# Kernel tuning notes

Measured on AMD Instinct MI355X. Metric: run time of the kernel, lower is better.

The kernel has to match this reference:

```python
import jax, jax.numpy as jnp
import numpy as np

B, T, V, E, H, NT = 64, 512, 8000, 256, 512, 4
HD = H // 2  # hidden per direction


def setup_inputs() -> dict:
    key = jax.random.key(0)
    ks = jax.random.split(key, 14)
    s = 0.1
    length = jnp.sort(jax.random.randint(ks[0], (B,), T // 2, T + 1))[::-1]  # sorted desc (pack_padded)
    mask = (jnp.arange(T)[None, :] < length[:, None]).astype(jnp.int32)
    sentence = jax.random.randint(ks[1], (B, T), 1, V + 1) * mask  # pad positions -> padding_idx 0
    tags = jax.random.randint(ks[2], (B, T), 0, NT)
    embedding = (jax.random.normal(ks[3], (V + 1, E)) * s).at[0].set(0.0)  # padding_idx row = 0
    w_ih_f = jax.random.normal(ks[4], (4 * HD, E)) * s
    w_hh_f = jax.random.normal(ks[5], (4 * HD, HD)) * s
    b_f = jax.random.normal(ks[6], (4 * HD,)) * s  # b_ih + b_hh combined
    w_ih_b = jax.random.normal(ks[7], (4 * HD, E)) * s
    w_hh_b = jax.random.normal(ks[8], (4 * HD, HD)) * s
    b_b = jax.random.normal(ks[9], (4 * HD,)) * s
    w_out = jax.random.normal(ks[10], (NT, H)) * s
    b_out = jnp.zeros((NT,), jnp.float32)
    start_trans = jax.random.uniform(ks[11], (NT,), minval=-0.1, maxval=0.1)
    end_trans = jax.random.uniform(ks[12], (NT,), minval=-0.1, maxval=0.1)
    trans = jax.random.uniform(ks[13], (NT, NT), minval=-0.1, maxval=0.1)
    return {"sentence": sentence, "tags": tags, "mask": mask, "length": length,
            "embedding": embedding, "w_ih_f": w_ih_f, "w_hh_f": w_hh_f, "b_f": b_f,
            "w_ih_b": w_ih_b, "w_hh_b": w_hh_b, "b_b": b_b,
            "w_out": w_out, "b_out": b_out,
            "start_trans": start_trans, "end_trans": end_trans, "trans": trans}


def _lstm_dir(x, maskf, w_ih, w_hh, b, reverse):
    # x: [B,T,E]; masked LSTM == packed LSTM (zero init state, padded outputs = 0)
    xg = jnp.einsum('bte,ge->btg', x, w_ih) + b           # [B,T,4HD]
    xg = jnp.swapaxes(xg, 0, 1)                           # [T,B,4HD]
    mt = jnp.swapaxes(maskf, 0, 1)[..., None]             # [T,B,1]
    h0 = jnp.zeros((x.shape[0], w_hh.shape[1]), x.dtype)

    def step(carry, inp):
        h, c = carry
        g, m = inp
        gates = g + h @ w_hh.T
        i, f, gg, o = jnp.split(gates, 4, axis=-1)  # torch gate order: i, f, g, o
        i = jax.nn.sigmoid(i); f = jax.nn.sigmoid(f)
        gg = jnp.tanh(gg); o = jax.nn.sigmoid(o)
        cn = f * c + i * gg
        hn = o * jnp.tanh(cn)
        h = m * hn + (1.0 - m) * h
        c = m * cn + (1.0 - m) * c
        return (h, c), h * m

    _, hs = jax.lax.scan(step, (h0, h0), (xg, mt), reverse=reverse)
    return jnp.swapaxes(hs, 0, 1)  # [B,T,HD]


def reference(sentence, tags, mask, length, embedding, w_ih_f, w_hh_f, b_f,
              w_ih_b, w_hh_b, b_b, w_out, b_out, start_trans, end_trans, trans):
    maskf = mask.astype(embedding.dtype)
    embeds = embedding[sentence]                           # [B,T,E] (dropout: eval/identity)
    hf = _lstm_dir(embeds, maskf, w_ih_f, w_hh_f, b_f, False)
    hb = _lstm_dir(embeds, maskf, w_ih_b, w_hh_b, b_b, True)
    feats = jnp.concatenate([hf, hb], -1) @ w_out.T + b_out  # [B,T,NT]

    # --- CRF log-likelihood (torchcrf), reduction='mean'; loss = -mean llh ---
    bsz = tags.shape[0]
    emit = jnp.take_along_axis(feats, tags[..., None], -1)[..., 0]   # [B,T]
    trans_sc = trans[tags[:, :-1], tags[:, 1:]]                       # [B,T-1]
    num = start_trans[tags[:, 0]] + emit[:, 0] \
        + jnp.sum(maskf[:, 1:] * (emit[:, 1:] + trans_sc), axis=1)
    last_tag = tags[jnp.arange(bsz), length - 1]
    num = num + end_trans[last_tag]

    ft = jnp.swapaxes(feats, 0, 1)                  # [T,B,NT]
    mt = jnp.swapaxes(maskf, 0, 1)[..., None]       # [T,B,1]
    alpha0 = start_trans[None, :] + ft[0]

    def step(alpha, inp):
        e, m = inp
        new = jax.nn.logsumexp(alpha[:, :, None] + trans[None] + e[:, None, :], axis=1)
        return m * new + (1.0 - m) * alpha, None

    alpha, _ = jax.lax.scan(step, alpha0, (ft[1:], mt[1:]))
    logZ = jax.nn.logsumexp(alpha + end_trans[None, :], axis=1)
    return -jnp.mean(num - logZ)
```

## Files before the change

### kernel.cpp

```cpp
#include <hip/hip_runtime.h>
#include <stdint.h>

#define BB 64
#define TT 512
#define EE 256
#define NTAG 4

typedef _Float16 f16;
typedef _Float16 half8 __attribute__((ext_vector_type(8)));
typedef _Float16 f16x4 __attribute__((ext_vector_type(4)));
typedef float floatx4 __attribute__((ext_vector_type(4)));

__device__ __forceinline__ int dot4i8(uint32_t a, uint32_t b, int c) {
#if __has_builtin(__builtin_amdgcn_sdot4)
  return __builtin_amdgcn_sdot4((int)a, (int)b, c, false);
#else
  int r;
  asm("v_dot4_i32_i8 %0, %1, %2, %3" : "=v"(r) : "v"(a), "v"(b), "v"(c));
  return r;
#endif
}

__device__ __forceinline__ float sigm(float x) {
  x = fminf(fmaxf(x, -30.f), 30.f);
  return 1.f / (1.f + __expf(-x));
}
__device__ __forceinline__ float tanh_f(float x) {
  x = fminf(fmaxf(x, -15.f), 15.f);
  float e = __expf(-2.f * x);
  return (1.f - e) / (1.f + e);
}

__global__ void pack_kernel(const float* __restrict__ wihf, const float* __restrict__ wihb,
                            const float* __restrict__ whhf, const float* __restrict__ whhb,
                            f16* __restrict__ bmat, uint32_t* __restrict__ whhp,
                            float* __restrict__ swhh) {
  int wv = (blockIdx.x * 256 + threadIdx.x) >> 6;
  int lane = threadIdx.x & 63;
  if (wv >= 2048) return;
  int dir = wv >> 10;
  int outr = wv & 1023;
  int srcg = (outr & 3) * 256 + (outr >> 2);
  const float* wih = dir ? wihb : wihf;
  const float* src = wih + (size_t)srcg * EE + lane * 4;
  f16* bp = bmat + (size_t)wv * EE + lane * 4;
  floatx4 v = *(const floatx4*)src;
  bp[0] = (f16)v[0]; bp[1] = (f16)v[1]; bp[2] = (f16)v[2]; bp[3] = (f16)v[3];
  int g = outr;
  const float* whh = dir ? whhb : whhf;
  floatx4 w = *(const floatx4*)(whh + (size_t)g * EE + lane * 4);
  float am = fmaxf(fmaxf(fabsf(w[0]), fabsf(w[1])), fmaxf(fabsf(w[2]), fabsf(w[3])));
#pragma unroll
  for (int d = 1; d < 64; d <<= 1) am = fmaxf(am, __shfl_xor(am, d));
  float s = am * (1.f / 127.f);
  float inv = am > 0.f ? 127.f / am : 0.f;
  int q0 = (int)rintf(w[0] * inv);
  int q1 = (int)rintf(w[1] * inv);
  int q2 = (int)rintf(w[2] * inv);
  int q3 = (int)rintf(w[3] * inv);
  uint32_t p = (uint32_t)(q0 & 255) | ((uint32_t)(q1 & 255) << 8) |
               ((uint32_t)(q2 & 255) << 16) | ((uint32_t)(q3 & 255) << 24);
  whhp[dir * 65536 + lane * 1024 + g] = p;
  if (lane == 0) swhh[dir * 1024 + g] = s;
}

__global__ __launch_bounds__(256) void gemm_kernel(
    const int* __restrict__ sentence, const float* __restrict__ embedding,
    const f16* __restrict__ bmat, f16* __restrict__ xgF, f16* __restrict__ xgB,
    int t0f, int t0b, int L, int Lsh) {
  __shared__ __attribute__((aligned(16))) f16 As[128][72];
  __shared__ __attribute__((aligned(16))) f16 Bs[128][72];
  int rt = blockIdx.x;
  int nt = blockIdx.y;
  int tid = threadIdx.x;
  int lane = tid & 63;
  int wv = tid >> 6;
  int BL = BB * L;
  int rbase = rt * 128;
  int half = (rbase >= BL) ? 1 : 0;
  int rloc0 = rbase - half * BL;
  int t0 = half ? t0b : t0f;

  floatx4 acc[4][4];
#pragma unroll
  for (int i = 0; i < 4; ++i)
#pragma unroll
    for (int j = 0; j < 4; ++j) acc[i][j] = (floatx4){0.f, 0.f, 0.f, 0.f};

  int ar = tid >> 1;
  int part = tid & 1;
  int rl = rloc0 + ar;
  int b_ = rl >> Lsh;
  int dt = rl & (L - 1);
  int t_ = t0 + dt;
  int sidx = sentence[b_ * TT + t_];
  const float* arow = embedding + (size_t)sidx * EE + part * 32;
  const f16* brow = bmat + ((size_t)(half * 1024 + nt * 128 + ar)) * EE + part * 32;
  int wm = (wv >> 1) * 64, wn = (wv & 1) * 64;

  for (int kk = 0; kk < 4; ++kk) {
    int k0 = kk * 64;
#pragma unroll
    for (int i = 0; i < 4; ++i) {
      floatx4 a0 = *(const floatx4*)(arow + k0 + i * 8);
      floatx4 a1 = *(const floatx4*)(arow + k0 + i * 8 + 4);
      union { f16 h[8]; uint4 u; } cv;
      cv.h[0] = (f16)a0[0]; cv.h[1] = (f16)a0[1]; cv.h[2] = (f16)a0[2]; cv.h[3] = (f16)a0[3];
      cv.h[4] = (f16)a1[0]; cv.h[5] = (f16)a1[1]; cv.h[6] = (f16)a1[2]; cv.h[7] = (f16)a1[3];
      *(uint4*)(&As[ar][part * 32 + i * 8]) = cv.u;
    }
#pragma unroll
    for (int i = 0; i < 4; ++i) {
      uint4 bv = *(const uint4*)(brow + k0 + i * 8);
      *(uint4*)(&Bs[ar][part * 32 + i * 8]) = bv;
    }
    __syncthreads();
#pragma unroll
    for (int kf = 0; kf < 2; ++kf) {
      int ko = kf * 32 + (lane >> 4) * 8;
      half8 af[4], bf[4];
#pragma unroll
      for (int mi = 0; mi < 4; ++mi)
        af[mi] = *(const half8*)(&As[wm + mi * 16 + (lane & 15)][ko]);
#pragma unroll
      for (int ni = 0; ni < 4; ++ni)
        bf[ni] = *(const half8*)(&Bs[wn + ni * 16 + (lane & 15)][ko]);
#pragma unroll
      for (int mi = 0; mi < 4; ++mi)
#pragma unroll
        for (int ni = 0; ni < 4; ++ni)
          acc[mi][ni] = __builtin_amdgcn_mfma_f32_16x16x32_f16(af[mi], bf[ni], acc[mi][ni], 0, 0, 0);
    }
    __syncthreads();
  }
  f16* out = half ? xgB : xgF;
#pragma unroll
  for (int mi = 0; mi < 4; ++mi) {
#pragma unroll
    for (int ni = 0; ni < 4; ++ni) {
      int rowl = wm + mi * 16 + (lane >> 4) * 4;
      int coll = nt * 128 + wn + ni * 16 + (lane & 15);
#pragma unroll
      for (int r = 0; r < 4; ++r) {
        out[(size_t)(rloc0 + rowl + r) * 1024 + coll] = (f16)acc[mi][ni][r];
      }
    }
  }
}

__global__ __launch_bounds__(256, 1) void rec_kernel(
    const int* __restrict__ length, const f16* __restrict__ xgF, const f16* __restrict__ xgB,
    const uint32_t* __restrict__ whhp, const float* __restrict__ swhh,
    const float* __restrict__ b_f, const float* __restrict__ b_b,
    f16* __restrict__ hsF, f16* __restrict__ hsB,
    float* __restrict__ hstate, float* __restrict__ cstate,
    int t0f, int t0b, int L, int first) {
  __shared__ __attribute__((aligned(16))) uint32_t hq4[2][64];
  int wid = blockIdx.x;
  int b = wid >> 1, dir = wid & 1;
  int j = threadIdx.x;
  int len = length[b];

  const uint32_t* wp = whhp + dir * 65536;
  uint32_t wr0[64], wr1[64], wr2[64], wr3[64];
#pragma unroll
  for (int q = 0; q < 64; ++q) {
    wr0[q] = wp[q * 1024 + j];
    wr1[q] = wp[q * 1024 + 256 + j];
    wr2[q] = wp[q * 1024 + 512 + j];
    wr3[q] = wp[q * 1024 + 768 + j];
  }
  const float* sb = swhh + dir * 1024;
  float sw0 = sb[j] * (1.f / 127.f), sw1 = sb[256 + j] * (1.f / 127.f);
  float sw2 = sb[512 + j] * (1.f / 127.f), sw3 = sb[768 + j] * (1.f / 127.f);
  const float* bias = dir ? b_b : b_f;
  float bi0 = bias[j], bi1 = bias[256 + j], bi2 = bias[512 + j], bi3 = bias[768 + j];

  float h = 0.f, c = 0.f;
  if (!first) {
    h = hstate[(dir * BB + b) * 256 + j];
    c = cstate[(dir * BB + b) * 256 + j];
  }
  const f16* xg = dir ? xgB : xgF;
  f16* hs = dir ? hsB : hsF;

  int qi = (int)rintf(h * 127.f);
  qi = max(-127, min(127, qi));
  ((uint8_t*)&hq4[0][0])[j] = (uint8_t)qi;
  __syncthreads();

  int tlo = dir ? t0b : t0f;
  int thi = min(tlo + L, len);
  int nsteps = thi - tlo;
  int p = 0;
  for (int ii = 0; ii < nsteps; ++ii) {
    int t = dir ? (thi - 1 - ii) : (tlo + ii);
    f16x4 xv = *(const f16x4*)(xg + (((size_t)(b * L + (t - tlo))) << 10) + j * 4);
    int A00 = 0, A01 = 0, A10 = 0, A11 = 0, A20 = 0, A21 = 0, A30 = 0, A31 = 0;
#pragma unroll
    for (int k = 0; k < 16; ++k) {
      uint4 v = *((const uint4*)&hq4[p][0] + k);
      A00 = dot4i8(wr0[4 * k + 0], v.x, A00); A01 = dot4i8(wr0[4 * k + 1], v.y, A01);
      A00 = dot4i8(wr0[4 * k + 2], v.z, A00); A01 = dot4i8(wr0[4 * k + 3], v.w, A01);
      A10 = dot4i8(wr1[4 * k + 0], v.x, A10); A11 = dot4i8(wr1[4 * k + 1], v.y, A11);
      A10 = dot4i8(wr1[4 * k + 2], v.z, A10); A11 = dot4i8(wr1[4 * k + 3], v.w, A11);
      A20 = dot4i8(wr2[4 * k + 0], v.x, A20); A21 = dot4i8(wr2[4 * k + 1], v.y, A21);
      A20 = dot4i8(wr2[4 * k + 2], v.z, A20); A21 = dot4i8(wr2[4 * k + 3], v.w, A21);
      A30 = dot4i8(wr3[4 * k + 0], v.x, A30); A31 = dot4i8(wr3[4 * k + 1], v.y, A31);
      A30 = dot4i8(wr3[4 * k + 2], v.z, A30); A31 = dot4i8(wr3[4 * k + 3], v.w, A31);
    }
    float pi = (float)xv[0] + bi0 + sw0 * (float)(A00 + A01);
    float pf = (float)xv[1] + bi1 + sw1 * (float)(A10 + A11);
    float pg = (float)xv[2] + bi2 + sw2 * (float)(A20 + A21);
    float po = (float)xv[3] + bi3 + sw3 * (float)(A30 + A31);
    float iv = sigm(pi), fv = sigm(pf), gv = tanh_f(pg), ov = sigm(po);
    c = fv * c + iv * gv;
    h = ov * tanh_f(c);
    hs[(((size_t)(b * TT + t)) << 8) + j] = (f16)h;
    int q = (int)rintf(h * 127.f);
    q = max(-127, min(127, q));
    ((uint8_t*)&hq4[p ^ 1][0])[j] = (uint8_t)q;
    __syncthreads();
    p ^= 1;
  }
  hstate[(dir * BB + b) * 256 + j] = h;
  cstate[(dir * BB + b) * 256 + j] = c;
}

__global__ __launch_bounds__(256) void feats_kernel(
    const f16* __restrict__ hsF, const f16* __restrict__ hsB,
    const float* __restrict__ w_out, const float* __restrict__ b_out,
    float* __restrict__ feats) {
  int gw = (blockIdx.x * 256 + threadIdx.x) >> 6;
  int lane = threadIdx.x & 63;
  int nw = (gridDim.x * 256) >> 6;
  float w0[8], w1[8], w2[8], w3[8];
#pragma unroll
  for (int u = 0; u < 8; ++u) {
    w0[u] = w_out[0 * 512 + lane * 8 + u];
    w1[u] = w_out[1 * 512 + lane * 8 + u];
    w2[u] = w_out[2 * 512 + lane * 8 + u];
    w3[u] = w_out[3 * 512 + lane * 8 + u];
  }
  float bo0 = b_out[0], bo1 = b_out[1], bo2 = b_out[2], bo3 = b_out[3];
  const f16* src0 = (lane < 32) ? (hsF + lane * 8) : (hsB + (lane - 32) * 8);
  for (int row = gw; row < BB * TT; row += nw) {
    union { uint4 u; f16 h[8]; } hv;
    hv.u = *(const uint4*)(src0 + ((size_t)row << 8));
    float a0 = 0.f, a1 = 0.f, a2 = 0.f, a3 = 0.f;
#pragma unroll
    for (int u2 = 0; u2 < 8; ++u2) {
      float x = (float)hv.h[u2];
      a0 += x * w0[u2]; a1 += x * w1[u2]; a2 += x * w2[u2]; a3 += x * w3[u2];
    }
#pragma unroll
    for (int d = 1; d < 64; d <<= 1) {
      a0 += __shfl_xor(a0, d); a1 += __shfl_xor(a1, d);
      a2 += __shfl_xor(a2, d); a3 += __shfl_xor(a3, d);
    }
    if (lane == 0) {
      floatx4 o = {a0 + bo0, a1 + bo1, a2 + bo2, a3 + bo3};
      *(floatx4*)(feats + (size_t)row * 4) = o;
    }
  }
}

__global__ void crf_kernel(const int* __restrict__ tags, const int* __restrict__ length,
                           const float* __restrict__ feats,
                           const float* __restrict__ start_trans,
                           const float* __restrict__ end_trans, const float* __restrict__ trans,
                           float* __restrict__ res) {
  int b = blockIdx.x;
  int lane = threadIdx.x;
  int len = length[b];
  float tr0 = lane < 4 ? trans[0 * 4 + lane] : 0.f;
  float tr1 = lane < 4 ? trans[1 * 4 + lane] : 0.f;
  float tr2 = lane < 4 ? trans[2 * 4 + lane] : 0.f;
  float tr3 = lane < 4 ? trans[3 * 4 + lane] : 0.f;
  float treg = lane < 16 ? trans[lane] : 0.f;
  float st = lane < 4 ? start_trans[lane] : 0.f;
  float en = lane < 4 ? end_trans[lane] : 0.f;
  const int* tg = tags + b * TT;
  const float* fb = feats + (size_t)b * TT * 4;

  float e = lane < 4 ? fb[lane] : 0.f;
  int prev = tg[0];
  float alpha = st + e;
  float num = __shfl(st + e, prev);
#pragma unroll 2
  for (int t = 1; t < len; ++t) {
    float et = lane < 4 ? fb[t * 4 + lane] : 0.f;
    int cur = tg[t];
    float a0 = __shfl(alpha, 0), a1 = __shfl(alpha, 1), a2 = __shfl(alpha, 2), a3 = __shfl(alpha, 3);
    float v0 = a0 + tr0, v1 = a1 + tr1, v2 = a2 + tr2, v3 = a3 + tr3;
    float mx = fmaxf(fmaxf(v0, v1), fmaxf(v2, v3));
    float sm = __expf(v0 - mx) + __expf(v1 - mx) + __expf(v2 - mx) + __expf(v3 - mx);
    alpha = mx + __logf(sm) + et;
    num += __shfl(et, cur) + __shfl(treg, prev * 4 + cur);
    prev = cur;
  }
  num += __shfl(en, prev);
  float v = alpha + en;
  float z0 = __shfl(v, 0), z1 = __shfl(v, 1), z2 = __shfl(v, 2), z3 = __shfl(v, 3);
  float mx = fmaxf(fmaxf(z0, z1), fmaxf(z2, z3));
  float logZ = mx + __logf(__expf(z0 - mx) + __expf(z1 - mx) + __expf(z2 - mx) + __expf(z3 - mx));
  if (lane == 0) res[b] = num - logZ;
}

__global__ void loss_kernel(const float* __restrict__ res, float* __restrict__ out) {
  int lane = threadIdx.x;
  float v = res[lane];
#pragma unroll
  for (int d = 1; d < 64; d <<= 1) v += __shfl_xor(v, d);
  if (lane == 0) out[0] = -v * (1.f / 64.f);
}

extern "C" void kernel_launch(void* const* d_in, const int* in_sizes, int n_in,
                              void* d_out, int out_size, void* d_ws, size_t ws_size,
                              hipStream_t stream) {
  (void)in_sizes; (void)n_in; (void)out_size;
  const int* sentence = (const int*)d_in[0];
  const int* tags = (const int*)d_in[1];
  const int* length = (const int*)d_in[3];
  const float* embedding = (const float*)d_in[4];
  const float* w_ih_f = (const float*)d_in[5];
  const float* w_hh_f = (const float*)d_in[6];
  const float* b_f = (const float*)d_in[7];
  const float* w_ih_b = (const float*)d_in[8];
  const float* w_hh_b = (const float*)d_in[9];
  const float* b_b = (const float*)d_in[10];
  const float* w_out = (const float*)d_in[11];
  const float* b_out = (const float*)d_in[12];
  const float* start_trans = (const float*)d_in[13];
  const float* end_trans = (const float*)d_in[14];
  const float* trans = (const float*)d_in[15];

  char* ws = (char*)d_ws;
  size_t off = 0;
  auto take = [&](size_t bytes) -> char* {
    char* p = ws + off;
    off = (off + bytes + 255) & ~(size_t)255;
    return p;
  };
  f16* bmat = (f16*)take((size_t)2048 * 256 * 2);
  uint32_t* whhp = (uint32_t*)take((size_t)2 * 64 * 1024 * 4);
  float* swhh = (float*)take((size_t)2 * 1024 * 4);
  f16* hsF = (f16*)take((size_t)BB * TT * 256 * 2);
  f16* hsB = (f16*)take((size_t)BB * TT * 256 * 2);
  float* feats = (float*)take((size_t)BB * TT * NTAG * 4);
  float* hstate = (float*)take((size_t)2 * BB * 256 * 4);
  float* cstate = (float*)take((size_t)2 * BB * 256 * 4);
  float* res = (float*)take(256);
  size_t fixed = off;

  int L = TT, Lsh = 9;
  while (L > 32 && fixed + (size_t)BB * L * 1024 * 2 * 2 > ws_size) { L >>= 1; Lsh--; }
  f16* xgF = (f16*)take((size_t)BB * L * 1024 * 2);
  f16* xgB = (f16*)take((size_t)BB * L * 1024 * 2);
  int NC = TT / L;

  hipLaunchKernelGGL(pack_kernel, dim3(512), dim3(256), 0, stream,
                     w_ih_f, w_ih_b, w_hh_f, w_hh_b, bmat, whhp, swhh);

  for (int cidx = 0; cidx < NC; ++cidx) {
    int t0f_ = cidx * L;
    int t0b_ = TT - (cidx + 1) * L;
    hipLaunchKernelGGL(gemm_kernel, dim3(2 * BB * L / 128, 8), dim3(256), 0, stream,
                       sentence, embedding, bmat, xgF, xgB, t0f_, t0b_, L, Lsh);
    hipLaunchKernelGGL(rec_kernel, dim3(128), dim3(256), 0, stream,
                       length, xgF, xgB, whhp, swhh, b_f, b_b, hsF, hsB,
                       hstate, cstate, t0f_, t0b_, L, cidx == 0 ? 1 : 0);
  }
  hipLaunchKernelGGL(feats_kernel, dim3(512), dim3(256), 0, stream,
                     hsF, hsB, w_out, b_out, feats);
  hipLaunchKernelGGL(crf_kernel, dim3(BB), dim3(64), 0, stream,
                     tags, length, feats, start_trans, end_trans, trans, res);
  hipLaunchKernelGGL(loss_kernel, dim3(1), dim3(64), 0, stream, res, (float*)d_out);
}
```

Measured before the change: 1.126 ms.

## Park recurrent weights in AGPRs and prefetch next-step input gates

```diff
diff --git a/kernel.cpp b/kernel.cpp
--- a/kernel.cpp
+++ b/kernel.cpp
@@ -8,7 +8,6 @@
 
 typedef _Float16 f16;
 typedef _Float16 half8 __attribute__((ext_vector_type(8)));
-typedef _Float16 f16x4 __attribute__((ext_vector_type(4)));
 typedef float floatx4 __attribute__((ext_vector_type(4)));
 
 __device__ __forceinline__ int dot4i8(uint32_t a, uint32_t b, int c) {
@@ -39,14 +38,12 @@
   int lane = threadIdx.x & 63;
   if (wv >= 2048) return;
   int dir = wv >> 10;
-  int outr = wv & 1023;
-  int srcg = (outr & 3) * 256 + (outr >> 2);
+  int g = wv & 1023;
   const float* wih = dir ? wihb : wihf;
-  const float* src = wih + (size_t)srcg * EE + lane * 4;
+  const float* src = wih + (size_t)g * EE + lane * 4;
   f16* bp = bmat + (size_t)wv * EE + lane * 4;
   floatx4 v = *(const floatx4*)src;
   bp[0] = (f16)v[0]; bp[1] = (f16)v[1]; bp[2] = (f16)v[2]; bp[3] = (f16)v[3];
-  int g = outr;
   const float* whh = dir ? whhb : whhf;
   floatx4 w = *(const floatx4*)(whh + (size_t)g * EE + lane * 4);
   float am = fmaxf(fmaxf(fabsf(w[0]), fabsf(w[1])), fmaxf(fabsf(w[2]), fabsf(w[3])));
@@ -85,7 +82,7 @@
 #pragma unroll
   for (int i = 0; i < 4; ++i)
 #pragma unroll
-    for (int j = 0; j < 4; ++j) acc[i][j] = (floatx4){0.f, 0.f, 0.f, 0.f};
+    for (int j2 = 0; j2 < 4; ++j2) acc[i][j2] = (floatx4){0.f, 0.f, 0.f, 0.f};
 
   int ar = tid >> 1;
   int part = tid & 1;
@@ -147,6 +144,58 @@
     }
   }
 }
+
+#define PARK4(c0, c1, c2, c3) \
+  uint32_t awI_##c0, awF_##c0, awG_##c0, awO_##c0; \
+  uint32_t awI_##c1, awF_##c1, awG_##c1, awO_##c1; \
+  uint32_t awI_##c2, awF_##c2, awG_##c2, awO_##c2; \
+  uint32_t awI_##c3, awF_##c3, awG_##c3, awO_##c3; \
+  { uint32_t xI0 = wp[(c0)*1024 + j],       xF0 = wp[(c0)*1024 + 256 + j]; \
+    uint32_t xG0 = wp[(c0)*1024 + 512 + j], xO0 = wp[(c0)*1024 + 768 + j]; \
+    uint32_t xI1 = wp[(c1)*1024 + j],       xF1 = wp[(c1)*1024 + 256 + j]; \
+    uint32_t xG1 = wp[(c1)*1024 + 512 + j], xO1 = wp[(c1)*1024 + 768 + j]; \
+    uint32_t xI2 = wp[(c2)*1024 + j],       xF2 = wp[(c2)*1024 + 256 + j]; \
+    uint32_t xG2 = wp[(c2)*1024 + 512 + j], xO2 = wp[(c2)*1024 + 768 + j]; \
+    uint32_t xI3 = wp[(c3)*1024 + j],       xF3 = wp[(c3)*1024 + 256 + j]; \
+    uint32_t xG3 = wp[(c3)*1024 + 512 + j], xO3 = wp[(c3)*1024 + 768 + j]; \
+    asm volatile("v_accvgpr_write_b32 %0, %1" : "=a"(awI_##c0) : "v"(xI0)); \
+    asm volatile("v_accvgpr_write_b32 %0, %1" : "=a"(awF_##c0) : "v"(xF0)); \
+    asm volatile("v_accvgpr_write_b32 %0, %1" : "=a"(awG_##c0) : "v"(xG0)); \
+    asm volatile("v_accvgpr_write_b32 %0, %1" : "=a"(awO_##c0) : "v"(xO0)); \
+    asm volatile("v_accvgpr_write_b32 %0, %1" : "=a"(awI_##c1) : "v"(xI1)); \
+    asm volatile("v_accvgpr_write_b32 %0, %1" : "=a"(awF_##c1) : "v"(xF1)); \
+    asm volatile("v_accvgpr_write_b32 %0, %1" : "=a"(awG_##c1) : "v"(xG1)); \
+    asm volatile("v_accvgpr_write_b32 %0, %1" : "=a"(awO_##c1) : "v"(xO1)); \
+    asm volatile("v_accvgpr_write_b32 %0, %1" : "=a"(awI_##c2) : "v"(xI2)); \
+    asm volatile("v_accvgpr_write_b32 %0, %1" : "=a"(awF_##c2) : "v"(xF2)); \
+    asm volatile("v_accvgpr_write_b32 %0, %1" : "=a"(awG_##c2) : "v"(xG2)); \
+    asm volatile("v_accvgpr_write_b32 %0, %1" : "=a"(awO_##c2) : "v"(xO2)); \
+    asm volatile("v_accvgpr_write_b32 %0, %1" : "=a"(awI_##c3) : "v"(xI3)); \
+    asm volatile("v_accvgpr_write_b32 %0, %1" : "=a"(awF_##c3) : "v"(xF3)); \
+    asm volatile("v_accvgpr_write_b32 %0, %1" : "=a"(awG_##c3) : "v"(xG3)); \
+    asm volatile("v_accvgpr_write_b32 %0, %1" : "=a"(awO_##c3) : "v"(xO3)); }
+
+#define RDW(nm) asm volatile("v_accvgpr_read_b32 %0, %1" : "=v"(w) : "a"(nm))
+
+#define DOTQ(q, c0, c1, c2, c3) { \
+  uint4 hv = hqcur[q]; \
+  uint32_t w; \
+  RDW(awI_##c0); Ai0 = dot4i8(w, hv.x, Ai0); \
+  RDW(awI_##c1); Ai1 = dot4i8(w, hv.y, Ai1); \
+  RDW(awI_##c2); Ai0 = dot4i8(w, hv.z, Ai0); \
+  RDW(awI_##c3); Ai1 = dot4i8(w, hv.w, Ai1); \
+  RDW(awF_##c0); Af0 = dot4i8(w, hv.x, Af0); \
+  RDW(awF_##c1); Af1 = dot4i8(w, hv.y, Af1); \
+  RDW(awF_##c2); Af0 = dot4i8(w, hv.z, Af0); \
+  RDW(awF_##c3); Af1 = dot4i8(w, hv.w, Af1); \
+  RDW(awG_##c0); Ag0 = dot4i8(w, hv.x, Ag0); \
+  RDW(awG_##c1); Ag1 = dot4i8(w, hv.y, Ag1); \
+  RDW(awG_##c2); Ag0 = dot4i8(w, hv.z, Ag0); \
+  RDW(awG_##c3); Ag1 = dot4i8(w, hv.w, Ag1); \
+  RDW(awO_##c0); Ao0 = dot4i8(w, hv.x, Ao0); \
+  RDW(awO_##c1); Ao1 = dot4i8(w, hv.y, Ao1); \
+  RDW(awO_##c2); Ao0 = dot4i8(w, hv.z, Ao0); \
+  RDW(awO_##c3); Ao1 = dot4i8(w, hv.w, Ao1); }
 
 __global__ __launch_bounds__(256, 1) void rec_kernel(
     const int* __restrict__ length, const f16* __restrict__ xgF, const f16* __restrict__ xgB,
@@ -162,19 +211,16 @@
   int len = length[b];
 
   const uint32_t* wp = whhp + dir * 65536;
-  uint32_t wr0[64], wr1[64], wr2[64], wr3[64];
-#pragma unroll
-  for (int q = 0; q < 64; ++q) {
-    wr0[q] = wp[q * 1024 + j];
-    wr1[q] = wp[q * 1024 + 256 + j];
-    wr2[q] = wp[q * 1024 + 512 + j];
-    wr3[q] = wp[q * 1024 + 768 + j];
-  }
+  PARK4(0, 1, 2, 3)     PARK4(4, 5, 6, 7)     PARK4(8, 9, 10, 11)   PARK4(12, 13, 14, 15)
+  PARK4(16, 17, 18, 19) PARK4(20, 21, 22, 23) PARK4(24, 25, 26, 27) PARK4(28, 29, 30, 31)
+  PARK4(32, 33, 34, 35) PARK4(36, 37, 38, 39) PARK4(40, 41, 42, 43) PARK4(44, 45, 46, 47)
+  PARK4(48, 49, 50, 51) PARK4(52, 53, 54, 55) PARK4(56, 57, 58, 59) PARK4(60, 61, 62, 63)
+
   const float* sb = swhh + dir * 1024;
-  float sw0 = sb[j] * (1.f / 127.f), sw1 = sb[256 + j] * (1.f / 127.f);
-  float sw2 = sb[512 + j] * (1.f / 127.f), sw3 = sb[768 + j] * (1.f / 127.f);
+  float swI = sb[j] * (1.f / 127.f), swF = sb[256 + j] * (1.f / 127.f);
+  float swG = sb[512 + j] * (1.f / 127.f), swO = sb[768 + j] * (1.f / 127.f);
   const float* bias = dir ? b_b : b_f;
-  float bi0 = bias[j], bi1 = bias[256 + j], bi2 = bias[512 + j], bi3 = bias[768 + j];
+  float biI = bias[j], biF = bias[256 + j], biG = bias[512 + j], biO = bias[768 + j];
 
   float h = 0.f, c = 0.f;
   if (!first) {
@@ -192,36 +238,43 @@
   int tlo = dir ? t0b : t0f;
   int thi = min(tlo + L, len);
   int nsteps = thi - tlo;
-  int p = 0;
+  int pp = 0;
+  int r0 = b * L + (dir ? (thi - 1 - tlo) : 0);
+  int sgn = dir ? -1 : 1;
+  f16 xI_c = (f16)0.f, xF_c = (f16)0.f, xG_c = (f16)0.f, xO_c = (f16)0.f;
+  if (nsteps > 0) {
+    const f16* xrow = xg + (((size_t)r0) << 10);
+    xI_c = xrow[j]; xF_c = xrow[256 + j]; xG_c = xrow[512 + j]; xO_c = xrow[768 + j];
+  }
   for (int ii = 0; ii < nsteps; ++ii) {
-    int t = dir ? (thi - 1 - ii) : (tlo + ii);
-    f16x4 xv = *(const f16x4*)(xg + (((size_t)(b * L + (t - tlo))) << 10) + j * 4);
-    int A00 = 0, A01 = 0, A10 = 0, A11 = 0, A20 = 0, A21 = 0, A30 = 0, A31 = 0;
-#pragma unroll
-    for (int k = 0; k < 16; ++k) {
-      uint4 v = *((const uint4*)&hq4[p][0] + k);
-      A00 = dot4i8(wr0[4 * k + 0], v.x, A00); A01 = dot4i8(wr0[4 * k + 1], v.y, A01);
-      A00 = dot4i8(wr0[4 * k + 2], v.z, A00); A01 = dot4i8(wr0[4 * k + 3], v.w, A01);
-      A10 = dot4i8(wr1[4 * k + 0], v.x, A10); A11 = dot4i8(wr1[4 * k + 1], v.y, A11);
-      A10 = dot4i8(wr1[4 * k + 2], v.z, A10); A11 = dot4i8(wr1[4 * k + 3], v.w, A11);
-      A20 = dot4i8(wr2[4 * k + 0], v.x, A20); A21 = dot4i8(wr2[4 * k + 1], v.y, A21);
-      A20 = dot4i8(wr2[4 * k + 2], v.z, A20); A21 = dot4i8(wr2[4 * k + 3], v.w, A21);
-      A30 = dot4i8(wr3[4 * k + 0], v.x, A30); A31 = dot4i8(wr3[4 * k + 1], v.y, A31);
-      A30 = dot4i8(wr3[4 * k + 2], v.z, A30); A31 = dot4i8(wr3[4 * k + 3], v.w, A31);
-    }
-    float pi = (float)xv[0] + bi0 + sw0 * (float)(A00 + A01);
-    float pf = (float)xv[1] + bi1 + sw1 * (float)(A10 + A11);
-    float pg = (float)xv[2] + bi2 + sw2 * (float)(A20 + A21);
-    float po = (float)xv[3] + bi3 + sw3 * (float)(A30 + A31);
+    f16 xI_n = xI_c, xF_n = xF_c, xG_n = xG_c, xO_n = xO_c;
+    if (ii + 1 < nsteps) {
+      const f16* xrow = xg + (((size_t)(r0 + sgn * (ii + 1))) << 10);
+      xI_n = xrow[j]; xF_n = xrow[256 + j]; xG_n = xrow[512 + j]; xO_n = xrow[768 + j];
+    }
+    const uint4* hqcur = (const uint4*)&hq4[pp][0];
+    int Ai0 = 0, Ai1 = 0, Af0 = 0, Af1 = 0, Ag0 = 0, Ag1 = 0, Ao0 = 0, Ao1 = 0;
+    DOTQ(0, 0, 1, 2, 3)     DOTQ(1, 4, 5, 6, 7)     DOTQ(2, 8, 9, 10, 11)
+    DOTQ(3, 12, 13, 14, 15) DOTQ(4, 16, 17, 18, 19) DOTQ(5, 20, 21, 22, 23)
+    DOTQ(6, 24, 25, 26, 27) DOTQ(7, 28, 29, 30, 31) DOTQ(8, 32, 33, 34, 35)
+    DOTQ(9, 36, 37, 38, 39) DOTQ(10, 40, 41, 42, 43) DOTQ(11, 44, 45, 46, 47)
+    DOTQ(12, 48, 49, 50, 51) DOTQ(13, 52, 53, 54, 55) DOTQ(14, 56, 57, 58, 59)
+    DOTQ(15, 60, 61, 62, 63)
+    float pi = (float)xI_c + biI + swI * (float)(Ai0 + Ai1);
+    float pf = (float)xF_c + biF + swF * (float)(Af0 + Af1);
+    float pg = (float)xG_c + biG + swG * (float)(Ag0 + Ag1);
+    float po = (float)xO_c + biO + swO * (float)(Ao0 + Ao1);
     float iv = sigm(pi), fv = sigm(pf), gv = tanh_f(pg), ov = sigm(po);
     c = fv * c + iv * gv;
     h = ov * tanh_f(c);
-    hs[(((size_t)(b * TT + t)) << 8) + j] = (f16)h;
+    int tt = dir ? (thi - 1 - ii) : (tlo + ii);
+    hs[(((size_t)(b * TT + tt)) << 8) + j] = (f16)h;
     int q = (int)rintf(h * 127.f);
     q = max(-127, min(127, q));
-    ((uint8_t*)&hq4[p ^ 1][0])[j] = (uint8_t)q;
+    ((uint8_t*)&hq4[pp ^ 1][0])[j] = (uint8_t)q;
     __syncthreads();
-    p ^= 1;
+    pp ^= 1;
+    xI_c = xI_n; xF_c = xF_n; xG_c = xG_n; xO_c = xO_n;
   }
   hstate[(dir * BB + b) * 256 + j] = h;
   cstate[(dir * BB + b) * 256 + j] = c;
```

Measured after the change: 1.181 ms. 1.05x slower.

## Split each LSTM recurrence across two peer blocks with flag-based hidden exchange

Applied to the files above, without the earlier changes.

```diff
diff --git a/kernel.cpp b/kernel.cpp
--- a/kernel.cpp
+++ b/kernel.cpp
@@ -8,7 +8,6 @@
 
 typedef _Float16 f16;
 typedef _Float16 half8 __attribute__((ext_vector_type(8)));
-typedef _Float16 f16x4 __attribute__((ext_vector_type(4)));
 typedef float floatx4 __attribute__((ext_vector_type(4)));
 
 __device__ __forceinline__ int dot4i8(uint32_t a, uint32_t b, int c) {
@@ -34,19 +33,21 @@
 __global__ void pack_kernel(const float* __restrict__ wihf, const float* __restrict__ wihb,
                             const float* __restrict__ whhf, const float* __restrict__ whhb,
                             f16* __restrict__ bmat, uint32_t* __restrict__ whhp,
-                            float* __restrict__ swhh) {
+                            float* __restrict__ swhh, uint32_t* __restrict__ fl) {
+  if (blockIdx.x == 0) {
+    fl[threadIdx.x] = 0;
+    fl[256 + threadIdx.x] = 0;
+  }
   int wv = (blockIdx.x * 256 + threadIdx.x) >> 6;
   int lane = threadIdx.x & 63;
   if (wv >= 2048) return;
   int dir = wv >> 10;
-  int outr = wv & 1023;
-  int srcg = (outr & 3) * 256 + (outr >> 2);
+  int g = wv & 1023;
   const float* wih = dir ? wihb : wihf;
-  const float* src = wih + (size_t)srcg * EE + lane * 4;
+  const float* src = wih + (size_t)g * EE + lane * 4;
   f16* bp = bmat + (size_t)wv * EE + lane * 4;
   floatx4 v = *(const floatx4*)src;
   bp[0] = (f16)v[0]; bp[1] = (f16)v[1]; bp[2] = (f16)v[2]; bp[3] = (f16)v[3];
-  int g = outr;
   const float* whh = dir ? whhb : whhf;
   floatx4 w = *(const floatx4*)(whh + (size_t)g * EE + lane * 4);
   float am = fmaxf(fmaxf(fabsf(w[0]), fabsf(w[1])), fmaxf(fabsf(w[2]), fabsf(w[3])));
@@ -85,7 +86,7 @@
 #pragma unroll
   for (int i = 0; i < 4; ++i)
 #pragma unroll
-    for (int j = 0; j < 4; ++j) acc[i][j] = (floatx4){0.f, 0.f, 0.f, 0.f};
+    for (int j2 = 0; j2 < 4; ++j2) acc[i][j2] = (floatx4){0.f, 0.f, 0.f, 0.f};
 
   int ar = tid >> 1;
   int part = tid & 1;
@@ -148,83 +149,166 @@
   }
 }
 
+#define LDWO(k)  uint32_t wa##k = wpAo[(k)*1024];      uint32_t wb##k = wpBo[(k)*1024];
+#define LDWX(k)  uint32_t wa##k = wpAx[((k)-32)*1024]; uint32_t wb##k = wpBx[((k)-32)*1024];
+
+#define DOTQ4(k0,k1,k2,k3,HV) { uint4 hv = (HV); \
+  aA0 = dot4i8(wa##k0, hv.x, aA0); aA1 = dot4i8(wa##k1, hv.y, aA1); \
+  aA0 = dot4i8(wa##k2, hv.z, aA0); aA1 = dot4i8(wa##k3, hv.w, aA1); \
+  aB0 = dot4i8(wb##k0, hv.x, aB0); aB1 = dot4i8(wb##k1, hv.y, aB1); \
+  aB0 = dot4i8(wb##k2, hv.z, aB0); aB1 = dot4i8(wb##k3, hv.w, aB1); }
+
 __global__ __launch_bounds__(256, 1) void rec_kernel(
     const int* __restrict__ length, const f16* __restrict__ xgF, const f16* __restrict__ xgB,
     const uint32_t* __restrict__ whhp, const float* __restrict__ swhh,
     const float* __restrict__ b_f, const float* __restrict__ b_b,
     f16* __restrict__ hsF, f16* __restrict__ hsB,
     float* __restrict__ hstate, float* __restrict__ cstate,
+    uint32_t* __restrict__ hx, uint32_t* __restrict__ fl,
     int t0f, int t0b, int L, int first) {
-  __shared__ __attribute__((aligned(16))) uint32_t hq4[2][64];
-  int wid = blockIdx.x;
-  int b = wid >> 1, dir = wid & 1;
-  int j = threadIdx.x;
+  __shared__ __attribute__((aligned(16))) uint32_t hqd[64];
+  __shared__ float gbuf[128], obuf[128];
+
+  int bid = blockIdx.x;
+  int side = bid >> 7;
+  int sub = bid & 127;
+  int b = sub >> 1, dir = sub & 1;
+  int peer = bid ^ 128;
+  int tid = threadIdx.x;
+  int tl = tid & 127;
+  int grp = tid >> 7;
+  int dabs = side * 128 + tl;
+  int rowA = grp * 512 + dabs;
+  int rowB = rowA + 256;
   int len = length[b];
 
-  const uint32_t* wp = whhp + dir * 65536;
-  uint32_t wr0[64], wr1[64], wr2[64], wr3[64];
-#pragma unroll
-  for (int q = 0; q < 64; ++q) {
-    wr0[q] = wp[q * 1024 + j];
-    wr1[q] = wp[q * 1024 + 256 + j];
-    wr2[q] = wp[q * 1024 + 512 + j];
-    wr3[q] = wp[q * 1024 + 768 + j];
-  }
-  const float* sb = swhh + dir * 1024;
-  float sw0 = sb[j] * (1.f / 127.f), sw1 = sb[256 + j] * (1.f / 127.f);
-  float sw2 = sb[512 + j] * (1.f / 127.f), sw3 = sb[768 + j] * (1.f / 127.f);
+  const uint32_t* wpbase = whhp + dir * 65536;
+  const uint32_t* wpAo = wpbase + rowA + (size_t)(side * 32) * 1024;
+  const uint32_t* wpAx = wpbase + rowA + (size_t)((side ^ 1) * 32) * 1024;
+  const uint32_t* wpBo = wpbase + rowB + (size_t)(side * 32) * 1024;
+  const uint32_t* wpBx = wpbase + rowB + (size_t)((side ^ 1) * 32) * 1024;
+  LDWO(0)  LDWO(1)  LDWO(2)  LDWO(3)  LDWO(4)  LDWO(5)  LDWO(6)  LDWO(7)
+  LDWO(8)  LDWO(9)  LDWO(10) LDWO(11) LDWO(12) LDWO(13) LDWO(14) LDWO(15)
+  LDWO(16) LDWO(17) LDWO(18) LDWO(19) LDWO(20) LDWO(21) LDWO(22) LDWO(23)
+  LDWO(24) LDWO(25) LDWO(26) LDWO(27) LDWO(28) LDWO(29) LDWO(30) LDWO(31)
+  LDWX(32) LDWX(33) LDWX(34) LDWX(35) LDWX(36) LDWX(37) LDWX(38) LDWX(39)
+  LDWX(40) LDWX(41) LDWX(42) LDWX(43) LDWX(44) LDWX(45) LDWX(46) LDWX(47)
+  LDWX(48) LDWX(49) LDWX(50) LDWX(51) LDWX(52) LDWX(53) LDWX(54) LDWX(55)
+  LDWX(56) LDWX(57) LDWX(58) LDWX(59) LDWX(60) LDWX(61) LDWX(62) LDWX(63)
+
+  float sA = swhh[dir * 1024 + rowA] * (1.f / 127.f);
+  float sB = swhh[dir * 1024 + rowB] * (1.f / 127.f);
   const float* bias = dir ? b_b : b_f;
-  float bi0 = bias[j], bi1 = bias[256 + j], bi2 = bias[512 + j], bi3 = bias[768 + j];
+  float bA = bias[rowA], bB = bias[rowB];
 
   float h = 0.f, c = 0.f;
-  if (!first) {
-    h = hstate[(dir * BB + b) * 256 + j];
-    c = cstate[(dir * BB + b) * 256 + j];
+  if (!first && tid < 128) {
+    h = hstate[(dir * BB + b) * 256 + dabs];
+    c = cstate[(dir * BB + b) * 256 + dabs];
   }
   const f16* xg = dir ? xgB : xgF;
   f16* hs = dir ? hsB : hsF;
-
-  int qi = (int)rintf(h * 127.f);
-  qi = max(-127, min(127, qi));
-  ((uint8_t*)&hq4[0][0])[j] = (uint8_t)qi;
-  __syncthreads();
 
   int tlo = dir ? t0b : t0f;
   int thi = min(tlo + L, len);
   int nsteps = thi - tlo;
-  int p = 0;
-  for (int ii = 0; ii < nsteps; ++ii) {
-    int t = dir ? (thi - 1 - ii) : (tlo + ii);
-    f16x4 xv = *(const f16x4*)(xg + (((size_t)(b * L + (t - tlo))) << 10) + j * 4);
-    int A00 = 0, A01 = 0, A10 = 0, A11 = 0, A20 = 0, A21 = 0, A30 = 0, A31 = 0;
-#pragma unroll
-    for (int k = 0; k < 16; ++k) {
-      uint4 v = *((const uint4*)&hq4[p][0] + k);
-      A00 = dot4i8(wr0[4 * k + 0], v.x, A00); A01 = dot4i8(wr0[4 * k + 1], v.y, A01);
-      A00 = dot4i8(wr0[4 * k + 2], v.z, A00); A01 = dot4i8(wr0[4 * k + 3], v.w, A01);
-      A10 = dot4i8(wr1[4 * k + 0], v.x, A10); A11 = dot4i8(wr1[4 * k + 1], v.y, A11);
-      A10 = dot4i8(wr1[4 * k + 2], v.z, A10); A11 = dot4i8(wr1[4 * k + 3], v.w, A11);
-      A20 = dot4i8(wr2[4 * k + 0], v.x, A20); A21 = dot4i8(wr2[4 * k + 1], v.y, A21);
-      A20 = dot4i8(wr2[4 * k + 2], v.z, A20); A21 = dot4i8(wr2[4 * k + 3], v.w, A21);
-      A30 = dot4i8(wr3[4 * k + 0], v.x, A30); A31 = dot4i8(wr3[4 * k + 1], v.y, A31);
-      A30 = dot4i8(wr3[4 * k + 2], v.z, A30); A31 = dot4i8(wr3[4 * k + 3], v.w, A31);
-    }
-    float pi = (float)xv[0] + bi0 + sw0 * (float)(A00 + A01);
-    float pf = (float)xv[1] + bi1 + sw1 * (float)(A10 + A11);
-    float pg = (float)xv[2] + bi2 + sw2 * (float)(A20 + A21);
-    float po = (float)xv[3] + bi3 + sw3 * (float)(A30 + A31);
-    float iv = sigm(pi), fv = sigm(pf), gv = tanh_f(pg), ov = sigm(po);
-    c = fv * c + iv * gv;
-    h = ov * tanh_f(c);
-    hs[(((size_t)(b * TT + t)) << 8) + j] = (f16)h;
+
+  const uint4* hqO = ((const uint4*)hqd) + side * 8;
+  const uint4* hqX = ((const uint4*)hqd) + (side ^ 1) * 8;
+  uint32_t* hxMine = hx + (size_t)bid * 64;
+  uint32_t* hxPeer = hx + (size_t)peer * 64;
+  uint32_t* flMine = fl + bid * 2;
+  uint32_t* flPeer = fl + peer * 2;
+
+  if (tid < 128) {
     int q = (int)rintf(h * 127.f);
     q = max(-127, min(127, q));
-    ((uint8_t*)&hq4[p ^ 1][0])[j] = (uint8_t)q;
-    __syncthreads();
-    p ^= 1;
-  }
-  hstate[(dir * BB + b) * 256 + j] = h;
-  cstate[(dir * BB + b) * 256 + j] = c;
+    ((uint8_t*)hqd)[dabs] = (uint8_t)q;
+  }
+  __syncthreads();
+  if (nsteps > 0) {
+    if (tid < 32) {
+      uint32_t v = hqd[side * 32 + tid];
+      __hip_atomic_store(hxMine + tid, v, __ATOMIC_RELAXED, __HIP_MEMORY_SCOPE_AGENT);
+    }
+    __syncthreads();
+    if (tid == 0)
+      __hip_atomic_store(flMine, 1u, __ATOMIC_RELEASE, __HIP_MEMORY_SCOPE_AGENT);
+  }
+
+  int r0 = b * L + (dir ? (thi - 1 - tlo) : 0);
+  int sgn = dir ? -1 : 1;
+  f16 xA_c = (f16)0.f, xB_c = (f16)0.f;
+  if (nsteps > 0) {
+    const f16* xr = xg + (((size_t)r0) << 10);
+    xA_c = xr[rowA]; xB_c = xr[rowB];
+  }
+
+  for (int e = 0; e < nsteps; ++e) {
+    f16 xA_n = xA_c, xB_n = xB_c;
+    if (e + 1 < nsteps) {
+      const f16* xr = xg + (((size_t)(r0 + sgn * (e + 1))) << 10);
+      xA_n = xr[rowA]; xB_n = xr[rowB];
+    }
+    int aA0 = 0, aA1 = 0, aB0 = 0, aB1 = 0;
+    DOTQ4(0, 1, 2, 3, hqO[0])     DOTQ4(4, 5, 6, 7, hqO[1])
+    DOTQ4(8, 9, 10, 11, hqO[2])   DOTQ4(12, 13, 14, 15, hqO[3])
+    DOTQ4(16, 17, 18, 19, hqO[4]) DOTQ4(20, 21, 22, 23, hqO[5])
+    DOTQ4(24, 25, 26, 27, hqO[6]) DOTQ4(28, 29, 30, 31, hqO[7])
+    int p = e & 1;
+    if (tid < 32) {
+      uint32_t want = (uint32_t)(e + 1);
+      int guard = 0;
+      while (__hip_atomic_load(flPeer + p, __ATOMIC_ACQUIRE, __HIP_MEMORY_SCOPE_AGENT) != want) {
+        __builtin_amdgcn_s_sleep(1);
+        if (++guard > (1 << 24)) break;
+      }
+      uint32_t v = __hip_atomic_load(hxPeer + p * 32 + tid, __ATOMIC_RELAXED, __HIP_MEMORY_SCOPE_AGENT);
+      hqd[(side ^ 1) * 32 + tid] = v;
+    }
+    __syncthreads();
+    if (tid == 0)
+      __hip_atomic_store(flPeer + p, 0u, __ATOMIC_RELAXED, __HIP_MEMORY_SCOPE_AGENT);
+    DOTQ4(32, 33, 34, 35, hqX[0]) DOTQ4(36, 37, 38, 39, hqX[1])
+    DOTQ4(40, 41, 42, 43, hqX[2]) DOTQ4(44, 45, 46, 47, hqX[3])
+    DOTQ4(48, 49, 50, 51, hqX[4]) DOTQ4(52, 53, 54, 55, hqX[5])
+    DOTQ4(56, 57, 58, 59, hqX[6]) DOTQ4(60, 61, 62, 63, hqX[7])
+    float pA = (float)xA_c + bA + sA * (float)(aA0 + aA1);
+    float pB = (float)xB_c + bB + sB * (float)(aB0 + aB1);
+    if (tid >= 128) {
+      gbuf[tl] = tanh_f(pA);
+      obuf[tl] = sigm(pB);
+    }
+    __syncthreads();
+    if (tid < 128) {
+      float iv = sigm(pA), fv = sigm(pB);
+      float gv = gbuf[tl], ov = obuf[tl];
+      c = fv * c + iv * gv;
+      h = ov * tanh_f(c);
+      int tt = dir ? (thi - 1 - e) : (tlo + e);
+      hs[(((size_t)(b * TT + tt)) << 8) + dabs] = (f16)h;
+      int q = (int)rintf(h * 127.f);
+      q = max(-127, min(127, q));
+      ((uint8_t*)hqd)[dabs] = (uint8_t)q;
+    }
+    __syncthreads();
+    if (e + 1 < nsteps) {
+      if (tid < 32) {
+        uint32_t v = hqd[side * 32 + tid];
+        __hip_atomic_store(hxMine + ((e + 1) & 1) * 32 + tid, v, __ATOMIC_RELAXED,
+                           __HIP_MEMORY_SCOPE_AGENT);
+      }
+      __syncthreads();
+      if (tid == 0)
+        __hip_atomic_store(flMine + ((e + 1) & 1), (uint32_t)(e + 2), __ATOMIC_RELEASE,
+                           __HIP_MEMORY_SCOPE_AGENT);
+    }
+    xA_c = xA_n; xB_c = xB_n;
+  }
+  if (tid < 128) {
+    hstate[(dir * BB + b) * 256 + dabs] = h;
+    cstate[(dir * BB + b) * 256 + dabs] = c;
+  }
 }
 
 __global__ __launch_bounds__(256) void feats_kernel(
@@ -350,6 +434,8 @@
   float* feats = (float*)take((size_t)BB * TT * NTAG * 4);
   float* hstate = (float*)take((size_t)2 * BB * 256 * 4);
   float* cstate = (float*)take((size_t)2 * BB * 256 * 4);
+  uint32_t* hx = (uint32_t*)take((size_t)256 * 64 * 4);
+  uint32_t* fl = (uint32_t*)take((size_t)512 * 4);
   float* res = (float*)take(256);
   size_t fixed = off;
 
@@ -360,16 +446,16 @@
   int NC = TT / L;
 
   hipLaunchKernelGGL(pack_kernel, dim3(512), dim3(256), 0, stream,
-                     w_ih_f, w_ih_b, w_hh_f, w_hh_b, bmat, whhp, swhh);
+                     w_ih_f, w_ih_b, w_hh_f, w_hh_b, bmat, whhp, swhh, fl);
 
   for (int cidx = 0; cidx < NC; ++cidx) {
     int t0f_ = cidx * L;
     int t0b_ = TT - (cidx + 1) * L;
     hipLaunchKernelGGL(gemm_kernel, dim3(2 * BB * L / 128, 8), dim3(256), 0, stream,
                        sentence, embedding, bmat, xgF, xgB, t0f_, t0b_, L, Lsh);
-    hipLaunchKernelGGL(rec_kernel, dim3(128), dim3(256), 0, stream,
+    hipLaunchKernelGGL(rec_kernel, dim3(256), dim3(256), 0, stream,
                        length, xgF, xgB, whhp, swhh, b_f, b_b, hsF, hsB,
-                       hstate, cstate, t0f_, t0b_, L, cidx == 0 ? 1 : 0);
+                       hstate, cstate, hx, fl, t0f_, t0b_, L, cidx == 0 ? 1 : 0);
   }
   hipLaunchKernelGGL(feats_kernel, dim3(512), dim3(256), 0, stream,
                      hsF, hsB, w_out, b_out, feats);
```

Result: slower. 2.562 ms (+127.5%).

## Quantize recurrent weights to int4 nibbles and stage them in LDS

Applied to the files above, without the earlier changes.

```diff
diff --git a/kernel.cpp b/kernel.cpp
--- a/kernel.cpp
+++ b/kernel.cpp
@@ -5,10 +5,10 @@
 #define TT 512
 #define EE 256
 #define NTAG 4
+#define SMEM_BYTES (131072 + 512 + 64)
 
 typedef _Float16 f16;
 typedef _Float16 half8 __attribute__((ext_vector_type(8)));
-typedef _Float16 f16x4 __attribute__((ext_vector_type(4)));
 typedef float floatx4 __attribute__((ext_vector_type(4)));
 
 __device__ __forceinline__ int dot4i8(uint32_t a, uint32_t b, int c) {
@@ -33,34 +33,35 @@
 
 __global__ void pack_kernel(const float* __restrict__ wihf, const float* __restrict__ wihb,
                             const float* __restrict__ whhf, const float* __restrict__ whhb,
-                            f16* __restrict__ bmat, uint32_t* __restrict__ whhp,
+                            f16* __restrict__ bmat, uint32_t* __restrict__ w4,
                             float* __restrict__ swhh) {
   int wv = (blockIdx.x * 256 + threadIdx.x) >> 6;
   int lane = threadIdx.x & 63;
   if (wv >= 2048) return;
   int dir = wv >> 10;
-  int outr = wv & 1023;
-  int srcg = (outr & 3) * 256 + (outr >> 2);
+  int g = wv & 1023;
   const float* wih = dir ? wihb : wihf;
-  const float* src = wih + (size_t)srcg * EE + lane * 4;
+  floatx4 v = *(const floatx4*)(wih + (size_t)g * EE + lane * 4);
   f16* bp = bmat + (size_t)wv * EE + lane * 4;
-  floatx4 v = *(const floatx4*)src;
   bp[0] = (f16)v[0]; bp[1] = (f16)v[1]; bp[2] = (f16)v[2]; bp[3] = (f16)v[3];
-  int g = outr;
+
   const float* whh = dir ? whhb : whhf;
   floatx4 w = *(const floatx4*)(whh + (size_t)g * EE + lane * 4);
   float am = fmaxf(fmaxf(fabsf(w[0]), fabsf(w[1])), fmaxf(fabsf(w[2]), fabsf(w[3])));
 #pragma unroll
   for (int d = 1; d < 64; d <<= 1) am = fmaxf(am, __shfl_xor(am, d));
-  float s = am * (1.f / 127.f);
-  float inv = am > 0.f ? 127.f / am : 0.f;
-  int q0 = (int)rintf(w[0] * inv);
-  int q1 = (int)rintf(w[1] * inv);
-  int q2 = (int)rintf(w[2] * inv);
-  int q3 = (int)rintf(w[3] * inv);
-  uint32_t p = (uint32_t)(q0 & 255) | ((uint32_t)(q1 & 255) << 8) |
-               ((uint32_t)(q2 & 255) << 16) | ((uint32_t)(q3 & 255) << 24);
-  whhp[dir * 65536 + lane * 1024 + g] = p;
+  float s = am * (1.f / 7.f);
+  float inv = am > 0.f ? 7.f / am : 0.f;
+  int q0 = max(-7, min(7, (int)rintf(w[0] * inv)));
+  int q1 = max(-7, min(7, (int)rintf(w[1] * inv)));
+  int q2 = max(-7, min(7, (int)rintf(w[2] * inv)));
+  int q3 = max(-7, min(7, (int)rintf(w[3] * inv)));
+  uint32_t n0 = (uint32_t)(q0 + 8), n1 = (uint32_t)(q1 + 8);
+  uint32_t n2 = (uint32_t)(q2 + 8), n3 = (uint32_t)(q3 + 8);
+  uint32_t hw = (lane & 1) ? ((n0 << 4) | (n1 << 12) | (n2 << 20) | (n3 << 28))
+                           : (n0 | (n1 << 8) | (n2 << 16) | (n3 << 24));
+  uint32_t other = __shfl_xor(hw, 1);
+  if (!(lane & 1)) w4[(size_t)dir * 32768 + (lane >> 1) * 1024 + g] = hw | other;
   if (lane == 0) swhh[dir * 1024 + g] = s;
 }
 
@@ -85,7 +86,7 @@
 #pragma unroll
   for (int i = 0; i < 4; ++i)
 #pragma unroll
-    for (int j = 0; j < 4; ++j) acc[i][j] = (floatx4){0.f, 0.f, 0.f, 0.f};
+    for (int j2 = 0; j2 < 4; ++j2) acc[i][j2] = (floatx4){0.f, 0.f, 0.f, 0.f};
 
   int ar = tid >> 1;
   int part = tid & 1;
@@ -150,31 +151,31 @@
 
 __global__ __launch_bounds__(256, 1) void rec_kernel(
     const int* __restrict__ length, const f16* __restrict__ xgF, const f16* __restrict__ xgB,
-    const uint32_t* __restrict__ whhp, const float* __restrict__ swhh,
+    const uint32_t* __restrict__ w4, const float* __restrict__ swhh,
     const float* __restrict__ b_f, const float* __restrict__ b_b,
     f16* __restrict__ hsF, f16* __restrict__ hsB,
     float* __restrict__ hstate, float* __restrict__ cstate,
     int t0f, int t0b, int L, int first) {
-  __shared__ __attribute__((aligned(16))) uint32_t hq4[2][64];
+  extern __shared__ uint32_t lds[];
+  uint32_t* wl = lds;
+  uint32_t* hq = lds + 32768;
+  int* sums = (int*)(lds + 32768 + 128);
+
   int wid = blockIdx.x;
   int b = wid >> 1, dir = wid & 1;
   int j = threadIdx.x;
+  int wv = j >> 6, lane = j & 63;
   int len = length[b];
 
-  const uint32_t* wp = whhp + dir * 65536;
-  uint32_t wr0[64], wr1[64], wr2[64], wr3[64];
-#pragma unroll
-  for (int q = 0; q < 64; ++q) {
-    wr0[q] = wp[q * 1024 + j];
-    wr1[q] = wp[q * 1024 + 256 + j];
-    wr2[q] = wp[q * 1024 + 512 + j];
-    wr3[q] = wp[q * 1024 + 768 + j];
-  }
+  const uint32_t* wg = w4 + (size_t)dir * 32768;
+#pragma unroll 4
+  for (int i = 0; i < 128; ++i) wl[i * 256 + j] = wg[i * 256 + j];
+
   const float* sb = swhh + dir * 1024;
-  float sw0 = sb[j] * (1.f / 127.f), sw1 = sb[256 + j] * (1.f / 127.f);
-  float sw2 = sb[512 + j] * (1.f / 127.f), sw3 = sb[768 + j] * (1.f / 127.f);
+  float swI = sb[j] * (1.f / 127.f), swF = sb[256 + j] * (1.f / 127.f);
+  float swG = sb[512 + j] * (1.f / 127.f), swO = sb[768 + j] * (1.f / 127.f);
   const float* bias = dir ? b_b : b_f;
-  float bi0 = bias[j], bi1 = bias[256 + j], bi2 = bias[512 + j], bi3 = bias[768 + j];
+  float biI = bias[j], biF = bias[256 + j], biG = bias[512 + j], biO = bias[768 + j];
 
   float h = 0.f, c = 0.f;
   if (!first) {
@@ -184,44 +185,73 @@
   const f16* xg = dir ? xgB : xgF;
   f16* hs = dir ? hsB : hsF;
 
-  int qi = (int)rintf(h * 127.f);
-  qi = max(-127, min(127, qi));
-  ((uint8_t*)&hq4[0][0])[j] = (uint8_t)qi;
+  {
+    int q = max(-127, min(127, (int)rintf(h * 127.f)));
+    ((uint8_t*)hq)[j] = (uint8_t)q;
+    int s = q;
+#pragma unroll
+    for (int d = 1; d < 64; d <<= 1) s += __shfl_xor(s, d);
+    if (lane == 0) sums[wv] = s;
+  }
   __syncthreads();
 
   int tlo = dir ? t0b : t0f;
   int thi = min(tlo + L, len);
   int nsteps = thi - tlo;
   int p = 0;
+  int r0 = b * L + (dir ? (thi - 1 - tlo) : 0);
+  int sgn = dir ? -1 : 1;
+  float xI_c = 0.f, xF_c = 0.f, xG_c = 0.f, xO_c = 0.f;
+  if (nsteps > 0) {
+    const f16* xr = xg + ((size_t)r0 << 10);
+    xI_c = (float)xr[j]; xF_c = (float)xr[256 + j];
+    xG_c = (float)xr[512 + j]; xO_c = (float)xr[768 + j];
+  }
+
   for (int ii = 0; ii < nsteps; ++ii) {
-    int t = dir ? (thi - 1 - ii) : (tlo + ii);
-    f16x4 xv = *(const f16x4*)(xg + (((size_t)(b * L + (t - tlo))) << 10) + j * 4);
-    int A00 = 0, A01 = 0, A10 = 0, A11 = 0, A20 = 0, A21 = 0, A30 = 0, A31 = 0;
-#pragma unroll
-    for (int k = 0; k < 16; ++k) {
-      uint4 v = *((const uint4*)&hq4[p][0] + k);
-      A00 = dot4i8(wr0[4 * k + 0], v.x, A00); A01 = dot4i8(wr0[4 * k + 1], v.y, A01);
-      A00 = dot4i8(wr0[4 * k + 2], v.z, A00); A01 = dot4i8(wr0[4 * k + 3], v.w, A01);
-      A10 = dot4i8(wr1[4 * k + 0], v.x, A10); A11 = dot4i8(wr1[4 * k + 1], v.y, A11);
-      A10 = dot4i8(wr1[4 * k + 2], v.z, A10); A11 = dot4i8(wr1[4 * k + 3], v.w, A11);
-      A20 = dot4i8(wr2[4 * k + 0], v.x, A20); A21 = dot4i8(wr2[4 * k + 1], v.y, A21);
-      A20 = dot4i8(wr2[4 * k + 2], v.z, A20); A21 = dot4i8(wr2[4 * k + 3], v.w, A21);
-      A30 = dot4i8(wr3[4 * k + 0], v.x, A30); A31 = dot4i8(wr3[4 * k + 1], v.y, A31);
-      A30 = dot4i8(wr3[4 * k + 2], v.z, A30); A31 = dot4i8(wr3[4 * k + 3], v.w, A31);
-    }
-    float pi = (float)xv[0] + bi0 + sw0 * (float)(A00 + A01);
-    float pf = (float)xv[1] + bi1 + sw1 * (float)(A10 + A11);
-    float pg = (float)xv[2] + bi2 + sw2 * (float)(A20 + A21);
-    float po = (float)xv[3] + bi3 + sw3 * (float)(A30 + A31);
-    float iv = sigm(pi), fv = sigm(pf), gv = tanh_f(pg), ov = sigm(po);
+    float xI_n = xI_c, xF_n = xF_c, xG_n = xG_c, xO_n = xO_c;
+    if (ii + 1 < nsteps) {
+      const f16* xr = xg + ((size_t)(r0 + sgn * (ii + 1)) << 10);
+      xI_n = (float)xr[j]; xF_n = (float)xr[256 + j];
+      xG_n = (float)xr[512 + j]; xO_n = (float)xr[768 + j];
+    }
+    int corr = 8 * (sums[p * 4 + 0] + sums[p * 4 + 1] + sums[p * 4 + 2] + sums[p * 4 + 3]);
+    const uint32_t* hp = hq + p * 64;
+    int aI0 = 0, aI1 = 0, aF0 = 0, aF1 = 0, aG0 = 0, aG1 = 0, aO0 = 0, aO1 = 0;
+#pragma unroll
+    for (int kc = 0; kc < 32; ++kc) {
+      uint32_t hx = hp[2 * kc], hy = hp[2 * kc + 1];
+      uint32_t nI = wl[kc * 1024 + j];
+      uint32_t nF = wl[kc * 1024 + 256 + j];
+      uint32_t nG = wl[kc * 1024 + 512 + j];
+      uint32_t nO = wl[kc * 1024 + 768 + j];
+      aI0 = dot4i8(nI & 0x0F0F0F0Fu, hx, aI0);
+      aI1 = dot4i8((nI >> 4) & 0x0F0F0F0Fu, hy, aI1);
+      aF0 = dot4i8(nF & 0x0F0F0F0Fu, hx, aF0);
+      aF1 = dot4i8((nF >> 4) & 0x0F0F0F0Fu, hy, aF1);
+      aG0 = dot4i8(nG & 0x0F0F0F0Fu, hx, aG0);
+      aG1 = dot4i8((nG >> 4) & 0x0F0F0F0Fu, hy, aG1);
+      aO0 = dot4i8(nO & 0x0F0F0F0Fu, hx, aO0);
+      aO1 = dot4i8((nO >> 4) & 0x0F0F0F0Fu, hy, aO1);
+    }
+    float pI = xI_c + biI + swI * (float)(aI0 + aI1 - corr);
+    float pF = xF_c + biF + swF * (float)(aF0 + aF1 - corr);
+    float pG = xG_c + biG + swG * (float)(aG0 + aG1 - corr);
+    float pO = xO_c + biO + swO * (float)(aO0 + aO1 - corr);
+    float iv = sigm(pI), fv = sigm(pF), gv = tanh_f(pG), ov = sigm(pO);
     c = fv * c + iv * gv;
     h = ov * tanh_f(c);
+    int t = dir ? (thi - 1 - ii) : (tlo + ii);
     hs[(((size_t)(b * TT + t)) << 8) + j] = (f16)h;
-    int q = (int)rintf(h * 127.f);
-    q = max(-127, min(127, q));
-    ((uint8_t*)&hq4[p ^ 1][0])[j] = (uint8_t)q;
+    int qn = max(-127, min(127, (int)rintf(h * 127.f)));
+    ((uint8_t*)(hq + (p ^ 1) * 64))[j] = (uint8_t)qn;
+    int s2 = qn;
+#pragma unroll
+    for (int d = 1; d < 64; d <<= 1) s2 += __shfl_xor(s2, d);
+    if (lane == 0) sums[(p ^ 1) * 4 + wv] = s2;
     __syncthreads();
     p ^= 1;
+    xI_c = xI_n; xF_c = xF_n; xG_c = xG_n; xO_c = xO_n;
   }
   hstate[(dir * BB + b) * 256 + j] = h;
   cstate[(dir * BB + b) * 256 + j] = c;
@@ -335,6 +365,10 @@
   const float* end_trans = (const float*)d_in[14];
   const float* trans = (const float*)d_in[15];
 
+  static_assert(SMEM_BYTES <= 160 * 1024, "LDS overflow");
+  (void)hipFuncSetAttribute(reinterpret_cast<const void*>(rec_kernel),
+                            hipFuncAttributeMaxDynamicSharedMemorySize, SMEM_BYTES);
+
   char* ws = (char*)d_ws;
   size_t off = 0;
   auto take = [&](size_t bytes) -> char* {
@@ -343,7 +377,7 @@
     return p;
   };
   f16* bmat = (f16*)take((size_t)2048 * 256 * 2);
-  uint32_t* whhp = (uint32_t*)take((size_t)2 * 64 * 1024 * 4);
+  uint32_t* w4 = (uint32_t*)take((size_t)2 * 32768 * 4);
   float* swhh = (float*)take((size_t)2 * 1024 * 4);
   f16* hsF = (f16*)take((size_t)BB * TT * 256 * 2);
   f16* hsB = (f16*)take((size_t)BB * TT * 256 * 2);
@@ -360,15 +394,15 @@
   int NC = TT / L;
 
   hipLaunchKernelGGL(pack_kernel, dim3(512), dim3(256), 0, stream,
-                     w_ih_f, w_ih_b, w_hh_f, w_hh_b, bmat, whhp, swhh);
+                     w_ih_f, w_ih_b, w_hh_f, w_hh_b, bmat, w4, swhh);
 
   for (int cidx = 0; cidx < NC; ++cidx) {
     int t0f_ = cidx * L;
     int t0b_ = TT - (cidx + 1) * L;
     hipLaunchKernelGGL(gemm_kernel, dim3(2 * BB * L / 128, 8), dim3(256), 0, stream,
                        sentence, embedding, bmat, xgF, xgB, t0f_, t0b_, L, Lsh);
-    hipLaunchKernelGGL(rec_kernel, dim3(128), dim3(256), 0, stream,
-                       length, xgF, xgB, whhp, swhh, b_f, b_b, hsF, hsB,
+    hipLaunchKernelGGL(rec_kernel, dim3(128), dim3(256), SMEM_BYTES, stream,
+                       length, xgF, xgB, w4, swhh, b_f, b_b, hsF, hsB,
                        hstate, cstate, t0f_, t0b_, L, cidx == 0 ? 1 : 0);
   }
   hipLaunchKernelGGL(feats_kernel, dim3(512), dim3(256), 0, stream,
```

Result: slower. 1.579 ms (+40.3%).
